# Optimization experiments

Measured on AMD Instinct MI355X. Metric: run time of the kernel, lower is better.

## Reference

```python
import jax, jax.numpy as jnp
import numpy as np

V_F_LEN = 512
I_F_LEN = 256
F_LEN = V_F_LEN + I_F_LEN  # 768, GRU input_size == hidden_size == f_len
NUM_LAYERS = 2
B, S = 64, 256


def _uniform(key, shape, scale):
    return jax.random.uniform(key, shape, jnp.float32, -scale, scale)


def setup_inputs() -> dict:
    key = jax.random.key(0)
    ks = jax.random.split(key, 16)
    fv = jax.random.normal(ks[0], (B, S, V_F_LEN), jnp.float32)
    fi = jax.random.normal(ks[1], (B, S, I_F_LEN), jnp.float32)
    ts = jax.random.uniform(ks[2], (B, S), jnp.float32)
    H = F_LEN
    sc = 1.0 / np.sqrt(H)
    # GRU params, PyTorch layout: [num_layers, 3H, H] with gate order (r, z, n)
    W_ih = _uniform(ks[3], (NUM_LAYERS, 3 * H, H), sc)
    W_hh = _uniform(ks[4], (NUM_LAYERS, 3 * H, H), sc)
    b_ih = _uniform(ks[5], (NUM_LAYERS, 3 * H), sc)
    b_hh = _uniform(ks[6], (NUM_LAYERS, 3 * H), sc)
    sc1 = 1.0 / np.sqrt(H)
    sc2 = 1.0 / np.sqrt(128)
    W1 = _uniform(ks[7], (128, H), sc1)
    b1 = _uniform(ks[8], (128,), sc1)
    W2 = _uniform(ks[9], (6, 128), sc2)
    b2 = _uniform(ks[10], (6,), sc2)
    return {"fv": fv, "fi": fi, "ts": ts, "W_ih": W_ih, "W_hh": W_hh,
            "b_ih": b_ih, "b_hh": b_hh, "W1": W1, "b1": b1, "W2": W2, "b2": b2}


def _gru_layer(x, h0, Wih, Whh, bih, bhh):
    # x: [B, S, H], h0: [B, H]
    def step(h, x_t):
        gi = x_t @ Wih.T + bih          # [B, 3H]
        gh = h @ Whh.T + bhh
        ir, iz, in_ = jnp.split(gi, 3, axis=-1)
        hr, hz, hn = jnp.split(gh, 3, axis=-1)
        r = jax.nn.sigmoid(ir + hr)
        z = jax.nn.sigmoid(iz + hz)
        n = jnp.tanh(in_ + r * hn)
        h_new = (1.0 - z) * n + z * h
        return h_new, h_new
    h_last, ys = jax.lax.scan(step, h0, jnp.swapaxes(x, 0, 1))  # ys: [S, B, H]
    return jnp.swapaxes(ys, 0, 1), h_last


def reference(fv, fi, ts, W_ih, W_hh, b_ih, b_hh, W1, b1, W2, b2):
    # FusionModule with fuse_method='cat': concatenate along feature dim
    fused = jnp.concatenate([fv, fi], axis=-1)  # [B, S, F_LEN]
    bsz = fused.shape[0]
    h0 = jnp.zeros((NUM_LAYERS, bsz, F_LEN), fused.dtype)
    # Note: the torch module feeds one timestep at a time, but the math is
    # identical to running the full sequence through the multilayer GRU.
    x = fused
    h_finals = []
    for l in range(NUM_LAYERS):
        x, h_l = _gru_layer(x, h0[l], W_ih[l], W_hh[l], b_ih[l], b_hh[l])
        h_finals.append(h_l)
    h_n = jnp.stack(h_finals, axis=0)  # [L, B, H]
    hdn = x @ W1.T + b1
    hdn = jnp.where(hdn >= 0, hdn, 0.1 * hdn)  # LeakyReLU(0.1)
    pose = hdn @ W2.T + b2                      # [B, S, 6]
    return (pose, h_n)
```

## Files before the change

kernel.cpp:

```cpp
#include <hip/hip_runtime.h>
#include <stdint.h>


typedef __attribute__((ext_vector_type(8))) short bf16x8;
typedef __attribute__((ext_vector_type(4))) short bf16x4;
typedef __attribute__((ext_vector_type(4))) float f32x4;

#define H_   768
#define TH3  2304
#define BATCH 64
#define SEQ  256
#define SLAB (BATCH * H_)
#define WROW 772
#define FL_ROUND 512

__device__ __forceinline__ uint16_t f2b(float f) {
  union { float f; uint32_t u; } v; v.f = f;
  uint32_t u = v.u;
  return (uint16_t)((u + 0x7FFFu + ((u >> 16) & 1u)) >> 16);
}

__device__ __forceinline__ f32x4 mfma16(bf16x8 a, bf16x8 b, f32x4 c) {
  return __builtin_amdgcn_mfma_f32_16x16x32_bf16(a, b, c, 0, 0, 0);
}

__device__ __forceinline__ bf16x8 ldB(const uint16_t* p) {
  bf16x4 lo = *reinterpret_cast<const bf16x4*>(p);
  bf16x4 hi = *reinterpret_cast<const bf16x4*>(p + 4);
  bf16x8 r;
  r[0] = lo[0]; r[1] = lo[1]; r[2] = lo[2]; r[3] = lo[3];
  r[4] = hi[0]; r[5] = hi[1]; r[6] = hi[2]; r[7] = hi[3];
  return r;
}

__device__ __forceinline__ int fidx(int i, int m, int grp, int slice) {
  return ((i * 2 + m) * 4 + grp) * 64 + slice;
}

__device__ __forceinline__ void pollFlags(const int* base, int lane) {
  const int* fp = base + (lane < 48 ? lane : 0);
  int spins = 0;
  for (;;) {
    int v = __hip_atomic_load(fp, __ATOMIC_RELAXED, __HIP_MEMORY_SCOPE_AGENT);
    if (lane >= 48) v = 1;
    if (__all(v != 0)) break;
    if (++spins > (1 << 15)) break;
    __builtin_amdgcn_s_sleep(1);
  }
  __builtin_amdgcn_sched_barrier(0);
}

__global__ __launch_bounds__(256) void prep_kernel(
    const float* __restrict__ fv, const float* __restrict__ fi,
    const float* __restrict__ W1,
    uint16_t* __restrict__ Xbf, int* __restrict__ flags, uint16_t* __restrict__ W1b)
{
  const int NX = SEQ * SLAB;
  const int NC = 257 * FL_ROUND;
  const int NW = 128 * H_;
  const int total = NX + NC + NW;
  for (int idx = blockIdx.x * blockDim.x + threadIdx.x; idx < total;
       idx += gridDim.x * blockDim.x) {
    if (idx < NX) {
      int s = idx / SLAB;
      int rem = idx - s * SLAB;
      int b = rem / H_;
      int h = rem - b * H_;
      float val = (h < 512) ? fv[((size_t)b * SEQ + s) * 512 + h]
                            : fi[((size_t)b * SEQ + s) * 256 + (h - 512)];
      Xbf[idx] = f2b(val);
    } else if (idx < NX + NC) {
      flags[idx - NX] = 0;
    } else {
      int k = idx - NX - NC;
      W1b[k] = f2b(W1[k]);
    }
  }
}

__global__ __launch_bounds__(256) void gru_persist(
    const float* __restrict__ Wih, const float* __restrict__ Whh,
    const float* __restrict__ bih, const float* __restrict__ bhh,
    const uint16_t* __restrict__ Xbf, uint16_t* __restrict__ Y0, uint16_t* __restrict__ Y1,
    int* __restrict__ flags, float* __restrict__ out_hn)
{
  __shared__ __attribute__((aligned(16))) uint16_t Wx[48 * WROW];
  __shared__ __attribute__((aligned(16))) uint16_t Wh[48 * WROW];
  __shared__ float ghbuf[2][32 * 48];
  __shared__ float hmast[32 * 16];
  __shared__ float bI[48];
  __shared__ float bH[48];

  const int bid   = blockIdx.x;
  const int slice = bid % 48;
  const int layer = (bid / 48) & 1;
  const int bhalf = bid / 96;
  const int grp   = bhalf * 2 + layer;
  const int tid  = threadIdx.x;
  const int lane = tid & 63;
  const int wid  = tid >> 6;
  const int mblk = wid & 1;
  const int isGh = wid >> 1;
  const int n16  = lane & 15;
  const int kg   = lane >> 4;

  const float* wx_g = Wih + (size_t)layer * TH3 * H_;
  const float* wh_g = Whh + (size_t)layer * TH3 * H_;
  for (int idx = tid; idx < 48 * H_; idx += 256) {
    int lr = idx / H_;
    int c  = idx - lr * H_;
    int gate = lr >> 4, j = lr & 15;
    size_t grow = (size_t)(gate * H_ + slice * 16 + j);
    Wx[lr * WROW + c] = f2b(wx_g[grow * H_ + c]);
    Wh[lr * WROW + c] = f2b(wh_g[grow * H_ + c]);
  }
  if (tid < 48) {
    int gate = tid >> 4, j = tid & 15;
    bI[tid] = bih[layer * TH3 + gate * H_ + slice * 16 + j];
    bH[tid] = bhh[layer * TH3 + gate * H_ + slice * 16 + j];
  }
  for (int idx = tid; idx < 32 * 16; idx += 256) hmast[idx] = 0.0f;
  __syncthreads();

  const int batch0 = bhalf * 32;
  uint16_t* Yown = layer ? Y1 : Y0;
  const uint16_t* Wl_h = Wh + (size_t)n16 * WROW + kg * 8;
  const uint16_t* Wl_x = Wx + (size_t)n16 * WROW + kg * 8;

  f32x4 xac0 = {0,0,0,0}, xac1 = {0,0,0,0}, xac2 = {0,0,0,0};

  for (int i = 0; i <= 256; ++i) {
    const bool active = (layer == 0) ? (i < 256) : (i >= 1);
    const bool firstA = (layer == 0) ? (i == 0) : (i == 1);
    float* gb = ghbuf[i & 1];

    if (active) {
      if (isGh) {
        if (firstA) {
          #pragma unroll
          for (int q = 0; q < 4; ++q) {
            int bi = mblk * 16 + 4 * kg + q;
            gb[bi * 48 +      n16] = 0.0f;
            gb[bi * 48 + 16 + n16] = 0.0f;
            gb[bi * 48 + 32 + n16] = 0.0f;
          }
        } else {
          pollFlags(flags + fidx(i - 1, mblk, grp, 0), lane);
          const uint16_t* hs = (layer == 0) ? (Y0 + (size_t)i * SLAB)
                                            : (Y1 + (size_t)(i - 1) * SLAB);
          const uint16_t* ap = hs + (size_t)(batch0 + mblk * 16 + n16) * H_ + kg * 8;
          f32x4 a0 = {0,0,0,0}, a1 = {0,0,0,0}, a2 = {0,0,0,0};
          #pragma unroll
          for (int ks = 0; ks < 24; ++ks) {
            bf16x8 av  = *reinterpret_cast<const bf16x8*>(ap + ks * 32);
            bf16x8 bv0 = ldB(Wl_h + ks * 32);
            bf16x8 bv1 = ldB(Wl_h + 16 * WROW + ks * 32);
            bf16x8 bv2 = ldB(Wl_h + 32 * WROW + ks * 32);
            a0 = mfma16(av, bv0, a0);
            a1 = mfma16(av, bv1, a1);
            a2 = mfma16(av, bv2, a2);
          }
          #pragma unroll
          for (int q = 0; q < 4; ++q) {
            int bi = mblk * 16 + 4 * kg + q;
            gb[bi * 48 +      n16] = a0[q];
            gb[bi * 48 + 16 + n16] = a1[q];
            gb[bi * 48 + 32 + n16] = a2[q];
          }
        }
      } else {
        if (layer == 1) pollFlags(flags + fidx(i - 1, mblk, bhalf * 2, 0), lane);
        const uint16_t* xs = (layer == 0) ? (Xbf + (size_t)i * SLAB)
                                          : (Y0 + (size_t)i * SLAB);
        const uint16_t* ap = xs + (size_t)(batch0 + mblk * 16 + n16) * H_ + kg * 8;
        f32x4 a0 = {0,0,0,0}, a1 = {0,0,0,0}, a2 = {0,0,0,0};
        #pragma unroll
        for (int ks = 0; ks < 24; ++ks) {
          bf16x8 av  = *reinterpret_cast<const bf16x8*>(ap + ks * 32);
          bf16x8 bv0 = ldB(Wl_x + ks * 32);
          bf16x8 bv1 = ldB(Wl_x + 16 * WROW + ks * 32);
          bf16x8 bv2 = ldB(Wl_x + 32 * WROW + ks * 32);
          a0 = mfma16(av, bv0, a0);
          a1 = mfma16(av, bv1, a1);
          a2 = mfma16(av, bv2, a2);
        }
        xac0 = a0; xac1 = a1; xac2 = a2;
      }
    }

    __syncthreads();

    if (active && !isGh) {
      uint16_t* dst = Yown + (size_t)((layer == 0) ? (i + 1) : i) * SLAB;
      const bool lastStep = (layer == 0) ? (i == 255) : (i == 256);
      #pragma unroll
      for (int q = 0; q < 4; ++q) {
        int bi = mblk * 16 + 4 * kg + q;
        float ghr = gb[bi * 48 +      n16] + bH[n16];
        float ghz = gb[bi * 48 + 16 + n16] + bH[16 + n16];
        float ghn = gb[bi * 48 + 32 + n16] + bH[32 + n16];
        float gxr = xac0[q] + bI[n16];
        float gxz = xac1[q] + bI[16 + n16];
        float gxn = xac2[q] + bI[32 + n16];
        float rg = 1.0f / (1.0f + __expf(-(gxr + ghr)));
        float zg = 1.0f / (1.0f + __expf(-(gxz + ghz)));
        float ng = tanhf(gxn + rg * ghn);
        float hv = hmast[bi * 16 + n16];
        float hn2 = (1.0f - zg) * ng + zg * hv;
        hmast[bi * 16 + n16] = hn2;
        uint32_t lo = (uint32_t)f2b(hn2);
        uint32_t partner = (uint32_t)__shfl_xor((int)lo, 1, 64);
        if ((n16 & 1) == 0) {
          uint32_t pack = lo | (partner << 16);
          uint32_t* p = (uint32_t*)(dst + (size_t)(batch0 + bi) * H_ + slice * 16 + n16);
          __hip_atomic_store(p, pack, __ATOMIC_RELAXED, __HIP_MEMORY_SCOPE_AGENT);
        }
        if (lastStep)
          out_hn[(size_t)layer * SLAB + (size_t)(batch0 + bi) * H_ + slice * 16 + n16] = hn2;
      }
      __builtin_amdgcn_s_waitcnt(0);
      __builtin_amdgcn_sched_barrier(0);
      if (lane == 0)
        __hip_atomic_store(&flags[fidx(i, mblk, grp, slice)], 1, __ATOMIC_RELAXED,
                           __HIP_MEMORY_SCOPE_AGENT);
    }
  }
}

__global__ __launch_bounds__(256) void regressor_kernel(
    const uint16_t* __restrict__ Y1, const uint16_t* __restrict__ W1b,
    const float* __restrict__ b1, const float* __restrict__ W2,
    const float* __restrict__ b2, float* __restrict__ pose)
{
  __shared__ float hdn[64 * 132];
  const int t = blockIdx.x;
  const int tid = threadIdx.x;
  const int lane = tid & 63;
  const int wid = tid >> 6;
  const int n16 = lane & 15;
  const int kg = lane >> 4;

  const uint16_t* A  = Y1 + (size_t)(t + 1) * SLAB + (size_t)(wid * 16) * H_;
  const uint16_t* ap = A + (size_t)n16 * H_ + kg * 8;
  const uint16_t* bp = W1b + (size_t)n16 * H_ + kg * 8;

  f32x4 acc[8];
  #pragma unroll
  for (int i = 0; i < 8; ++i) acc[i] = (f32x4){0,0,0,0};

  #pragma unroll
  for (int ks = 0; ks < 24; ++ks) {
    bf16x8 av = *reinterpret_cast<const bf16x8*>(ap + ks * 32);
    #pragma unroll
    for (int nt = 0; nt < 8; ++nt) {
      bf16x8 bv = *reinterpret_cast<const bf16x8*>(bp + (size_t)nt * 16 * H_ + ks * 32);
      acc[nt] = mfma16(av, bv, acc[nt]);
    }
  }
  #pragma unroll
  for (int nt = 0; nt < 8; ++nt) {
    #pragma unroll
    for (int q = 0; q < 4; ++q) {
      int brow = wid * 16 + 4 * kg + q;
      int col  = nt * 16 + n16;
      float v = acc[nt][q] + b1[col];
      v = (v >= 0.0f) ? v : 0.1f * v;
      hdn[brow * 132 + col] = v;
    }
  }
  __syncthreads();
  for (int idx = tid; idx < 384; idx += 256) {
    int b = idx / 6, o = idx % 6;
    const float* w2r = W2 + o * 128;
    const float* hr  = &hdn[b * 132];
    float s = b2[o];
    #pragma unroll 4
    for (int c = 0; c < 128; ++c) s += hr[c] * w2r[c];
    pose[(size_t)b * (SEQ * 6) + (size_t)t * 6 + o] = s;
  }
}

extern "C" void kernel_launch(void* const* d_in, const int* in_sizes, int n_in,
                              void* d_out, int out_size, void* d_ws, size_t ws_size,
                              hipStream_t stream) {
  const float* fv  = (const float*)d_in[0];
  const float* fi  = (const float*)d_in[1];
  const float* Wih = (const float*)d_in[3];
  const float* Whh = (const float*)d_in[4];
  const float* bih = (const float*)d_in[5];
  const float* bhh = (const float*)d_in[6];
  const float* W1  = (const float*)d_in[7];
  const float* b1  = (const float*)d_in[8];
  const float* W2  = (const float*)d_in[9];
  const float* b2  = (const float*)d_in[10];
  float* out = (float*)d_out;

  char* ws = (char*)d_ws;
  size_t off = 0;
  int* flags = (int*)(ws + off);
  off += (size_t)257 * FL_ROUND * sizeof(int);
  off = (off + 255) & ~(size_t)255;
  uint16_t* Xbf = (uint16_t*)(ws + off); off += (size_t)SEQ * SLAB * 2;
  uint16_t* Y0  = (uint16_t*)(ws + off); off += (size_t)257 * SLAB * 2;
  uint16_t* Y1  = (uint16_t*)(ws + off); off += (size_t)257 * SLAB * 2;
  uint16_t* W1b = (uint16_t*)(ws + off); off += (size_t)128 * H_ * 2;

  prep_kernel<<<2048, 256, 0, stream>>>(fv, fi, W1, Xbf, flags, W1b);
  gru_persist<<<192, 256, 0, stream>>>(Wih, Whh, bih, bhh, Xbf, Y0, Y1, flags, out + 98304);
  regressor_kernel<<<SEQ, 256, 0, stream>>>(Y1, W1b, b1, W2, b2, out);
}
```

Baseline: 2.391 ms.

## Pack step flags into bytes, split hidden GEMM along K, use fast tanh

Per-step completion flags become bytes packed into 128-byte groups, so one wave polls all 96 producer slices with two byte loads per lane. Polling no longer sleeps and its spin limit is raised. The recurrent h·Whh GEMM is now split along K across the two Gh waves, each covering both 16-row batch blocks, and the gate stage sums the two partial results. This drops the ghbuf double buffer and reduces the flag wait on the critical path. tanhf is replaced by a clamped exp-based tanh, and removing the double buffer may add a shared-memory hazard between iterations.

Result: slower. 2.510 ms (+5.0%).

```diff
diff --git a/kernel.cpp b/kernel.cpp
--- a/kernel.cpp
+++ b/kernel.cpp
@@ -12,7 +12,7 @@
 #define SEQ  256
 #define SLAB (BATCH * H_)
 #define WROW 772
-#define FL_ROUND 512
+#define FB_ROUND 512
 
 __device__ __forceinline__ uint16_t f2b(float f) {
   union { float f; uint32_t u; } v; v.f = f;
@@ -33,21 +33,43 @@
   return r;
 }
 
-__device__ __forceinline__ int fidx(int i, int m, int grp, int slice) {
-  return ((i * 2 + m) * 4 + grp) * 64 + slice;
-}
-
-__device__ __forceinline__ void pollFlags(const int* base, int lane) {
-  const int* fp = base + (lane < 48 ? lane : 0);
+__device__ __forceinline__ size_t fbIdx(int i, int grp) { return ((size_t)i * 4 + grp) * 128; }
+
+__device__ __forceinline__ uint8_t ldFlag(const uint8_t* p) {
+  return __hip_atomic_load(p, __ATOMIC_RELAXED, __HIP_MEMORY_SCOPE_AGENT);
+}
+
+__device__ __forceinline__ void pollFlags96(const uint8_t* base, int lane) {
+  const uint8_t* p0 = base + lane;
+  const uint8_t* p1 = base + 64 + (lane & 31);
   int spins = 0;
   for (;;) {
-    int v = __hip_atomic_load(fp, __ATOMIC_RELAXED, __HIP_MEMORY_SCOPE_AGENT);
-    if (lane >= 48) v = 1;
-    if (__all(v != 0)) break;
-    if (++spins > (1 << 15)) break;
-    __builtin_amdgcn_s_sleep(1);
+    uint8_t a = ldFlag(p0);
+    uint8_t b = (lane < 32) ? ldFlag(p1) : (uint8_t)1;
+    if (__all(a && b)) break;
+    if (++spins > (1 << 18)) break;
   }
   __builtin_amdgcn_sched_barrier(0);
+}
+
+__device__ __forceinline__ void pollFlags48(const uint8_t* base, int lane) {
+  const uint8_t* p0 = base + (lane < 48 ? lane : 0);
+  int spins = 0;
+  for (;;) {
+    uint8_t a = (lane < 48) ? ldFlag(p0) : (uint8_t)1;
+    if (__all(a)) break;
+    if (++spins > (1 << 18)) break;
+  }
+  __builtin_amdgcn_sched_barrier(0);
+}
+
+__device__ __forceinline__ float fsig(float x) {
+  return 1.0f / (1.0f + __expf(-x));
+}
+__device__ __forceinline__ float ftanh(float x) {
+  x = fminf(fmaxf(x, -15.0f), 15.0f);
+  float e = __expf(2.0f * x);
+  return (e - 1.0f) / (e + 1.0f);
 }
 
 __global__ __launch_bounds__(256) void prep_kernel(
@@ -56,7 +78,7 @@
     uint16_t* __restrict__ Xbf, int* __restrict__ flags, uint16_t* __restrict__ W1b)
 {
   const int NX = SEQ * SLAB;
-  const int NC = 257 * FL_ROUND;
+  const int NC = 257 * FB_ROUND / 4;
   const int NW = 128 * H_;
   const int total = NX + NC + NW;
   for (int idx = blockIdx.x * blockDim.x + threadIdx.x; idx < total;
@@ -82,11 +104,11 @@
     const float* __restrict__ Wih, const float* __restrict__ Whh,
     const float* __restrict__ bih, const float* __restrict__ bhh,
     const uint16_t* __restrict__ Xbf, uint16_t* __restrict__ Y0, uint16_t* __restrict__ Y1,
-    int* __restrict__ flags, float* __restrict__ out_hn)
+    uint8_t* __restrict__ fbytes, float* __restrict__ out_hn)
 {
   __shared__ __attribute__((aligned(16))) uint16_t Wx[48 * WROW];
   __shared__ __attribute__((aligned(16))) uint16_t Wh[48 * WROW];
-  __shared__ float ghbuf[2][32 * 48];
+  __shared__ float ghbuf[2 * 32 * 48];
   __shared__ float hmast[32 * 16];
   __shared__ float bI[48];
   __shared__ float bH[48];
@@ -99,8 +121,9 @@
   const int tid  = threadIdx.x;
   const int lane = tid & 63;
   const int wid  = tid >> 6;
+  const int isGh = wid >> 1;
   const int mblk = wid & 1;
-  const int isGh = wid >> 1;
+  const int kh   = wid & 1;
   const int n16  = lane & 15;
   const int kg   = lane >> 4;
 
@@ -124,52 +147,65 @@
 
   const int batch0 = bhalf * 32;
   uint16_t* Yown = layer ? Y1 : Y0;
-  const uint16_t* Wl_h = Wh + (size_t)n16 * WROW + kg * 8;
-  const uint16_t* Wl_x = Wx + (size_t)n16 * WROW + kg * 8;
+  const uint16_t* Wh_base = Wh + (size_t)n16 * WROW + kg * 8 + kh * 384;
+  const uint16_t* Wx_base = Wx + (size_t)n16 * WROW + kg * 8;
 
   f32x4 xac0 = {0,0,0,0}, xac1 = {0,0,0,0}, xac2 = {0,0,0,0};
 
   for (int i = 0; i <= 256; ++i) {
     const bool active = (layer == 0) ? (i < 256) : (i >= 1);
     const bool firstA = (layer == 0) ? (i == 0) : (i == 1);
-    float* gb = ghbuf[i & 1];
+    float* gb = ghbuf + kh * 1536;
 
     if (active) {
       if (isGh) {
         if (firstA) {
           #pragma unroll
           for (int q = 0; q < 4; ++q) {
-            int bi = mblk * 16 + 4 * kg + q;
-            gb[bi * 48 +      n16] = 0.0f;
-            gb[bi * 48 + 16 + n16] = 0.0f;
-            gb[bi * 48 + 32 + n16] = 0.0f;
+            #pragma unroll
+            for (int m = 0; m < 2; ++m) {
+              int bi = m * 16 + 4 * kg + q;
+              gb[bi * 48 +      n16] = 0.0f;
+              gb[bi * 48 + 16 + n16] = 0.0f;
+              gb[bi * 48 + 32 + n16] = 0.0f;
+            }
           }
         } else {
-          pollFlags(flags + fidx(i - 1, mblk, grp, 0), lane);
+          pollFlags96(fbytes + fbIdx(i - 1, grp), lane);
           const uint16_t* hs = (layer == 0) ? (Y0 + (size_t)i * SLAB)
                                             : (Y1 + (size_t)(i - 1) * SLAB);
-          const uint16_t* ap = hs + (size_t)(batch0 + mblk * 16 + n16) * H_ + kg * 8;
-          f32x4 a0 = {0,0,0,0}, a1 = {0,0,0,0}, a2 = {0,0,0,0};
+          const uint16_t* ap0 = hs + (size_t)(batch0 + n16) * H_ + kh * 384 + kg * 8;
+          const uint16_t* ap1 = ap0 + (size_t)16 * H_;
+          f32x4 a00 = {0,0,0,0}, a01 = {0,0,0,0}, a02 = {0,0,0,0};
+          f32x4 a10 = {0,0,0,0}, a11 = {0,0,0,0}, a12 = {0,0,0,0};
           #pragma unroll
-          for (int ks = 0; ks < 24; ++ks) {
-            bf16x8 av  = *reinterpret_cast<const bf16x8*>(ap + ks * 32);
-            bf16x8 bv0 = ldB(Wl_h + ks * 32);
-            bf16x8 bv1 = ldB(Wl_h + 16 * WROW + ks * 32);
-            bf16x8 bv2 = ldB(Wl_h + 32 * WROW + ks * 32);
-            a0 = mfma16(av, bv0, a0);
-            a1 = mfma16(av, bv1, a1);
-            a2 = mfma16(av, bv2, a2);
+          for (int ks = 0; ks < 12; ++ks) {
+            bf16x8 av0 = *reinterpret_cast<const bf16x8*>(ap0 + ks * 32);
+            bf16x8 av1 = *reinterpret_cast<const bf16x8*>(ap1 + ks * 32);
+            bf16x8 bv0 = ldB(Wh_base + ks * 32);
+            bf16x8 bv1 = ldB(Wh_base + 16 * WROW + ks * 32);
+            bf16x8 bv2 = ldB(Wh_base + 32 * WROW + ks * 32);
+            a00 = mfma16(av0, bv0, a00);
+            a01 = mfma16(av0, bv1, a01);
+            a02 = mfma16(av0, bv2, a02);
+            a10 = mfma16(av1, bv0, a10);
+            a11 = mfma16(av1, bv1, a11);
+            a12 = mfma16(av1, bv2, a12);
           }
           #pragma unroll
           for (int q = 0; q < 4; ++q) {
-            int bi = mblk * 16 + 4 * kg + q;
-            gb[bi * 48 +      n16] = a0[q];
-            gb[bi * 48 + 16 + n16] = a1[q];
-            gb[bi * 48 + 32 + n16] = a2[q];
+            int bi0 = 4 * kg + q;
+            gb[bi0 * 48 +      n16] = a00[q];
+            gb[bi0 * 48 + 16 + n16] = a01[q];
+            gb[bi0 * 48 + 32 + n16] = a02[q];
+            int bi1 = 16 + bi0;
+            gb[bi1 * 48 +      n16] = a10[q];
+            gb[bi1 * 48 + 16 + n16] = a11[q];
+            gb[bi1 * 48 + 32 + n16] = a12[q];
           }
         }
       } else {
-        if (layer == 1) pollFlags(flags + fidx(i - 1, mblk, bhalf * 2, 0), lane);
+        if (layer == 1) pollFlags48(fbytes + fbIdx(i - 1, bhalf * 2) + mblk * 48, lane);
         const uint16_t* xs = (layer == 0) ? (Xbf + (size_t)i * SLAB)
                                           : (Y0 + (size_t)i * SLAB);
         const uint16_t* ap = xs + (size_t)(batch0 + mblk * 16 + n16) * H_ + kg * 8;
@@ -177,9 +213,9 @@
         #pragma unroll
         for (int ks = 0; ks < 24; ++ks) {
           bf16x8 av  = *reinterpret_cast<const bf16x8*>(ap + ks * 32);
-          bf16x8 bv0 = ldB(Wl_x + ks * 32);
-          bf16x8 bv1 = ldB(Wl_x + 16 * WROW + ks * 32);
-          bf16x8 bv2 = ldB(Wl_x + 32 * WROW + ks * 32);
+          bf16x8 bv0 = ldB(Wx_base + ks * 32);
+          bf16x8 bv1 = ldB(Wx_base + 16 * WROW + ks * 32);
+          bf16x8 bv2 = ldB(Wx_base + 32 * WROW + ks * 32);
           a0 = mfma16(av, bv0, a0);
           a1 = mfma16(av, bv1, a1);
           a2 = mfma16(av, bv2, a2);
@@ -196,15 +232,15 @@
       #pragma unroll
       for (int q = 0; q < 4; ++q) {
         int bi = mblk * 16 + 4 * kg + q;
-        float ghr = gb[bi * 48 +      n16] + bH[n16];
-        float ghz = gb[bi * 48 + 16 + n16] + bH[16 + n16];
-        float ghn = gb[bi * 48 + 32 + n16] + bH[32 + n16];
+        float ghr = ghbuf[bi * 48 +      n16] + ghbuf[1536 + bi * 48 +      n16] + bH[n16];
+        float ghz = ghbuf[bi * 48 + 16 + n16] + ghbuf[1536 + bi * 48 + 16 + n16] + bH[16 + n16];
+        float ghn = ghbuf[bi * 48 + 32 + n16] + ghbuf[1536 + bi * 48 + 32 + n16] + bH[32 + n16];
         float gxr = xac0[q] + bI[n16];
         float gxz = xac1[q] + bI[16 + n16];
         float gxn = xac2[q] + bI[32 + n16];
-        float rg = 1.0f / (1.0f + __expf(-(gxr + ghr)));
-        float zg = 1.0f / (1.0f + __expf(-(gxz + ghz)));
-        float ng = tanhf(gxn + rg * ghn);
+        float rg = fsig(gxr + ghr);
+        float zg = fsig(gxz + ghz);
+        float ng = ftanh(gxn + rg * ghn);
         float hv = hmast[bi * 16 + n16];
         float hn2 = (1.0f - zg) * ng + zg * hv;
         hmast[bi * 16 + n16] = hn2;
@@ -221,8 +257,8 @@
       __builtin_amdgcn_s_waitcnt(0);
       __builtin_amdgcn_sched_barrier(0);
       if (lane == 0)
-        __hip_atomic_store(&flags[fidx(i, mblk, grp, slice)], 1, __ATOMIC_RELAXED,
-                           __HIP_MEMORY_SCOPE_AGENT);
+        __hip_atomic_store(fbytes + fbIdx(i, grp) + mblk * 48 + slice, (uint8_t)1,
+                           __ATOMIC_RELAXED, __HIP_MEMORY_SCOPE_AGENT);
     }
   }
 }
@@ -297,15 +333,15 @@
 
   char* ws = (char*)d_ws;
   size_t off = 0;
-  int* flags = (int*)(ws + off);
-  off += (size_t)257 * FL_ROUND * sizeof(int);
+  uint8_t* fbytes = (uint8_t*)(ws + off);
+  off += (size_t)257 * FB_ROUND;
   off = (off + 255) & ~(size_t)255;
   uint16_t* Xbf = (uint16_t*)(ws + off); off += (size_t)SEQ * SLAB * 2;
   uint16_t* Y0  = (uint16_t*)(ws + off); off += (size_t)257 * SLAB * 2;
   uint16_t* Y1  = (uint16_t*)(ws + off); off += (size_t)257 * SLAB * 2;
   uint16_t* W1b = (uint16_t*)(ws + off); off += (size_t)128 * H_ * 2;
 
-  prep_kernel<<<2048, 256, 0, stream>>>(fv, fi, W1, Xbf, flags, W1b);
-  gru_persist<<<192, 256, 0, stream>>>(Wih, Whh, bih, bhh, Xbf, Y0, Y1, flags, out + 98304);
+  prep_kernel<<<2048, 256, 0, stream>>>(fv, fi, W1, Xbf, (int*)fbytes, W1b);
+  gru_persist<<<192, 256, 0, stream>>>(Wih, Whh, bih, bhh, Xbf, Y0, Y1, fbytes, out + 98304);
   regressor_kernel<<<SEQ, 256, 0, stream>>>(Y1, W1b, b1, W2, b2, out);
 }
```

## Merge batch halves into one 512-thread block per slice with block-level flags

Applied to the files above, without the earlier changes.

Each block now handles all 64 batch rows with 8 waves instead of two blocks each doing 32 rows, halving the grid from 192 to 96 blocks. Per-wave flags are replaced by one flag per block, published after a second block-wide barrier. The single-buffered gh scratch is now protected by that barrier, and the hidden state is kept in registers instead of shared memory. Custom fast sigmoid and tanh replace tanhf. This removes duplicated weight staging and cuts the number of flags each poll must check, at the cost of an extra barrier per step and less parallelism across CUs.

Result: no change. 2.348 ms (-1.8%).

```diff
diff --git a/kernel.cpp b/kernel.cpp
--- a/kernel.cpp
+++ b/kernel.cpp
@@ -12,7 +12,7 @@
 #define SEQ  256
 #define SLAB (BATCH * H_)
 #define WROW 772
-#define FL_ROUND 512
+#define FL_STRIDE 128
 
 __device__ __forceinline__ uint16_t f2b(float f) {
   union { float f; uint32_t u; } v; v.f = f;
@@ -33,21 +33,26 @@
   return r;
 }
 
-__device__ __forceinline__ int fidx(int i, int m, int grp, int slice) {
-  return ((i * 2 + m) * 4 + grp) * 64 + slice;
-}
-
-__device__ __forceinline__ void pollFlags(const int* base, int lane) {
+__device__ __forceinline__ void pollFlags48(const int* base, int lane) {
   const int* fp = base + (lane < 48 ? lane : 0);
   int spins = 0;
   for (;;) {
     int v = __hip_atomic_load(fp, __ATOMIC_RELAXED, __HIP_MEMORY_SCOPE_AGENT);
     if (lane >= 48) v = 1;
     if (__all(v != 0)) break;
-    if (++spins > (1 << 15)) break;
+    if (++spins > (1 << 16)) break;
     __builtin_amdgcn_s_sleep(1);
   }
   __builtin_amdgcn_sched_barrier(0);
+}
+
+__device__ __forceinline__ float fsig(float x) {
+  return 1.0f / (1.0f + __expf(-x));
+}
+__device__ __forceinline__ float ftanh(float x) {
+  x = fminf(fmaxf(x, -15.0f), 15.0f);
+  float e = __expf(2.0f * x);
+  return (e - 1.0f) / (e + 1.0f);
 }
 
 __global__ __launch_bounds__(256) void prep_kernel(
@@ -56,7 +61,7 @@
     uint16_t* __restrict__ Xbf, int* __restrict__ flags, uint16_t* __restrict__ W1b)
 {
   const int NX = SEQ * SLAB;
-  const int NC = 257 * FL_ROUND;
+  const int NC = 257 * FL_STRIDE;
   const int NW = 128 * H_;
   const int total = NX + NC + NW;
   for (int idx = blockIdx.x * blockDim.x + threadIdx.x; idx < total;
@@ -78,7 +83,7 @@
   }
 }
 
-__global__ __launch_bounds__(256) void gru_persist(
+__global__ __launch_bounds__(512) void gru_persist(
     const float* __restrict__ Wih, const float* __restrict__ Whh,
     const float* __restrict__ bih, const float* __restrict__ bhh,
     const uint16_t* __restrict__ Xbf, uint16_t* __restrict__ Y0, uint16_t* __restrict__ Y1,
@@ -86,27 +91,24 @@
 {
   __shared__ __attribute__((aligned(16))) uint16_t Wx[48 * WROW];
   __shared__ __attribute__((aligned(16))) uint16_t Wh[48 * WROW];
-  __shared__ float ghbuf[2][32 * 48];
-  __shared__ float hmast[32 * 16];
+  __shared__ float ghbuf[64 * 48];
   __shared__ float bI[48];
   __shared__ float bH[48];
 
   const int bid   = blockIdx.x;
   const int slice = bid % 48;
-  const int layer = (bid / 48) & 1;
-  const int bhalf = bid / 96;
-  const int grp   = bhalf * 2 + layer;
+  const int layer = bid / 48;
   const int tid  = threadIdx.x;
   const int lane = tid & 63;
   const int wid  = tid >> 6;
-  const int mblk = wid & 1;
-  const int isGh = wid >> 1;
+  const int isGh = wid >> 2;
+  const int mblk = wid & 3;
   const int n16  = lane & 15;
   const int kg   = lane >> 4;
 
   const float* wx_g = Wih + (size_t)layer * TH3 * H_;
   const float* wh_g = Whh + (size_t)layer * TH3 * H_;
-  for (int idx = tid; idx < 48 * H_; idx += 256) {
+  for (int idx = tid; idx < 48 * H_; idx += 512) {
     int lr = idx / H_;
     int c  = idx - lr * H_;
     int gate = lr >> 4, j = lr & 15;
@@ -119,20 +121,18 @@
     bI[tid] = bih[layer * TH3 + gate * H_ + slice * 16 + j];
     bH[tid] = bhh[layer * TH3 + gate * H_ + slice * 16 + j];
   }
-  for (int idx = tid; idx < 32 * 16; idx += 256) hmast[idx] = 0.0f;
   __syncthreads();
 
-  const int batch0 = bhalf * 32;
   uint16_t* Yown = layer ? Y1 : Y0;
-  const uint16_t* Wl_h = Wh + (size_t)n16 * WROW + kg * 8;
-  const uint16_t* Wl_x = Wx + (size_t)n16 * WROW + kg * 8;
+  const uint16_t* Wh_base = Wh + (size_t)n16 * WROW + kg * 8;
+  const uint16_t* Wx_base = Wx + (size_t)n16 * WROW + kg * 8;
 
   f32x4 xac0 = {0,0,0,0}, xac1 = {0,0,0,0}, xac2 = {0,0,0,0};
+  float hp[4] = {0.0f, 0.0f, 0.0f, 0.0f};
 
   for (int i = 0; i <= 256; ++i) {
     const bool active = (layer == 0) ? (i < 256) : (i >= 1);
     const bool firstA = (layer == 0) ? (i == 0) : (i == 1);
-    float* gb = ghbuf[i & 1];
 
     if (active) {
       if (isGh) {
@@ -140,22 +140,22 @@
           #pragma unroll
           for (int q = 0; q < 4; ++q) {
             int bi = mblk * 16 + 4 * kg + q;
-            gb[bi * 48 +      n16] = 0.0f;
-            gb[bi * 48 + 16 + n16] = 0.0f;
-            gb[bi * 48 + 32 + n16] = 0.0f;
+            ghbuf[bi * 48 +      n16] = 0.0f;
+            ghbuf[bi * 48 + 16 + n16] = 0.0f;
+            ghbuf[bi * 48 + 32 + n16] = 0.0f;
           }
         } else {
-          pollFlags(flags + fidx(i - 1, mblk, grp, 0), lane);
+          pollFlags48(flags + (size_t)(i - 1) * FL_STRIDE + layer * 64, lane);
           const uint16_t* hs = (layer == 0) ? (Y0 + (size_t)i * SLAB)
                                             : (Y1 + (size_t)(i - 1) * SLAB);
-          const uint16_t* ap = hs + (size_t)(batch0 + mblk * 16 + n16) * H_ + kg * 8;
+          const uint16_t* ap = hs + (size_t)(mblk * 16 + n16) * H_ + kg * 8;
           f32x4 a0 = {0,0,0,0}, a1 = {0,0,0,0}, a2 = {0,0,0,0};
           #pragma unroll
           for (int ks = 0; ks < 24; ++ks) {
             bf16x8 av  = *reinterpret_cast<const bf16x8*>(ap + ks * 32);
-            bf16x8 bv0 = ldB(Wl_h + ks * 32);
-            bf16x8 bv1 = ldB(Wl_h + 16 * WROW + ks * 32);
-            bf16x8 bv2 = ldB(Wl_h + 32 * WROW + ks * 32);
+            bf16x8 bv0 = ldB(Wh_base + ks * 32);
+            bf16x8 bv1 = ldB(Wh_base + 16 * WROW + ks * 32);
+            bf16x8 bv2 = ldB(Wh_base + 32 * WROW + ks * 32);
             a0 = mfma16(av, bv0, a0);
             a1 = mfma16(av, bv1, a1);
             a2 = mfma16(av, bv2, a2);
@@ -163,23 +163,23 @@
           #pragma unroll
           for (int q = 0; q < 4; ++q) {
             int bi = mblk * 16 + 4 * kg + q;
-            gb[bi * 48 +      n16] = a0[q];
-            gb[bi * 48 + 16 + n16] = a1[q];
-            gb[bi * 48 + 32 + n16] = a2[q];
+            ghbuf[bi * 48 +      n16] = a0[q];
+            ghbuf[bi * 48 + 16 + n16] = a1[q];
+            ghbuf[bi * 48 + 32 + n16] = a2[q];
           }
         }
       } else {
-        if (layer == 1) pollFlags(flags + fidx(i - 1, mblk, bhalf * 2, 0), lane);
+        if (layer == 1) pollFlags48(flags + (size_t)(i - 1) * FL_STRIDE, lane);
         const uint16_t* xs = (layer == 0) ? (Xbf + (size_t)i * SLAB)
                                           : (Y0 + (size_t)i * SLAB);
-        const uint16_t* ap = xs + (size_t)(batch0 + mblk * 16 + n16) * H_ + kg * 8;
+        const uint16_t* ap = xs + (size_t)(mblk * 16 + n16) * H_ + kg * 8;
         f32x4 a0 = {0,0,0,0}, a1 = {0,0,0,0}, a2 = {0,0,0,0};
         #pragma unroll
         for (int ks = 0; ks < 24; ++ks) {
           bf16x8 av  = *reinterpret_cast<const bf16x8*>(ap + ks * 32);
-          bf16x8 bv0 = ldB(Wl_x + ks * 32);
-          bf16x8 bv1 = ldB(Wl_x + 16 * WROW + ks * 32);
-          bf16x8 bv2 = ldB(Wl_x + 32 * WROW + ks * 32);
+          bf16x8 bv0 = ldB(Wx_base + ks * 32);
+          bf16x8 bv1 = ldB(Wx_base + 16 * WROW + ks * 32);
+          bf16x8 bv2 = ldB(Wx_base + 32 * WROW + ks * 32);
           a0 = mfma16(av, bv0, a0);
           a1 = mfma16(av, bv1, a1);
           a2 = mfma16(av, bv2, a2);
@@ -187,7 +187,6 @@
         xac0 = a0; xac1 = a1; xac2 = a2;
       }
     }
-
     __syncthreads();
 
     if (active && !isGh) {
@@ -196,34 +195,36 @@
       #pragma unroll
       for (int q = 0; q < 4; ++q) {
         int bi = mblk * 16 + 4 * kg + q;
-        float ghr = gb[bi * 48 +      n16] + bH[n16];
-        float ghz = gb[bi * 48 + 16 + n16] + bH[16 + n16];
-        float ghn = gb[bi * 48 + 32 + n16] + bH[32 + n16];
+        float ghr = ghbuf[bi * 48 +      n16] + bH[n16];
+        float ghz = ghbuf[bi * 48 + 16 + n16] + bH[16 + n16];
+        float ghn = ghbuf[bi * 48 + 32 + n16] + bH[32 + n16];
         float gxr = xac0[q] + bI[n16];
         float gxz = xac1[q] + bI[16 + n16];
         float gxn = xac2[q] + bI[32 + n16];
-        float rg = 1.0f / (1.0f + __expf(-(gxr + ghr)));
-        float zg = 1.0f / (1.0f + __expf(-(gxz + ghz)));
-        float ng = tanhf(gxn + rg * ghn);
-        float hv = hmast[bi * 16 + n16];
-        float hn2 = (1.0f - zg) * ng + zg * hv;
-        hmast[bi * 16 + n16] = hn2;
+        float rg = fsig(gxr + ghr);
+        float zg = fsig(gxz + ghz);
+        float ng = ftanh(gxn + rg * ghn);
+        float hn2 = (1.0f - zg) * ng + zg * hp[q];
+        hp[q] = hn2;
         uint32_t lo = (uint32_t)f2b(hn2);
         uint32_t partner = (uint32_t)__shfl_xor((int)lo, 1, 64);
         if ((n16 & 1) == 0) {
           uint32_t pack = lo | (partner << 16);
-          uint32_t* p = (uint32_t*)(dst + (size_t)(batch0 + bi) * H_ + slice * 16 + n16);
+          uint32_t* p = (uint32_t*)(dst + (size_t)bi * H_ + slice * 16 + n16);
           __hip_atomic_store(p, pack, __ATOMIC_RELAXED, __HIP_MEMORY_SCOPE_AGENT);
         }
         if (lastStep)
-          out_hn[(size_t)layer * SLAB + (size_t)(batch0 + bi) * H_ + slice * 16 + n16] = hn2;
+          out_hn[(size_t)layer * SLAB + (size_t)bi * H_ + slice * 16 + n16] = hn2;
       }
       __builtin_amdgcn_s_waitcnt(0);
       __builtin_amdgcn_sched_barrier(0);
-      if (lane == 0)
-        __hip_atomic_store(&flags[fidx(i, mblk, grp, slice)], 1, __ATOMIC_RELAXED,
-                           __HIP_MEMORY_SCOPE_AGENT);
-    }
+    }
+
+    __syncthreads();
+
+    if (i < 256 && tid == 0)
+      __hip_atomic_store(&flags[(size_t)i * FL_STRIDE + layer * 64 + slice], 1,
+                         __ATOMIC_RELAXED, __HIP_MEMORY_SCOPE_AGENT);
   }
 }
 
@@ -298,7 +299,7 @@
   char* ws = (char*)d_ws;
   size_t off = 0;
   int* flags = (int*)(ws + off);
-  off += (size_t)257 * FL_ROUND * sizeof(int);
+  off += (size_t)257 * FL_STRIDE * sizeof(int);
   off = (off + 255) & ~(size_t)255;
   uint16_t* Xbf = (uint16_t*)(ws + off); off += (size_t)SEQ * SLAB * 2;
   uint16_t* Y0  = (uint16_t*)(ws + off); off += (size_t)257 * SLAB * 2;
@@ -306,6 +307,6 @@
   uint16_t* W1b = (uint16_t*)(ws + off); off += (size_t)128 * H_ * 2;
 
   prep_kernel<<<2048, 256, 0, stream>>>(fv, fi, W1, Xbf, flags, W1b);
-  gru_persist<<<192, 256, 0, stream>>>(Wih, Whh, bih, bhh, Xbf, Y0, Y1, flags, out + 98304);
+  gru_persist<<<96, 512, 0, stream>>>(Wih, Whh, bih, bhh, Xbf, Y0, Y1, flags, out + 98304);
   regressor_kernel<<<SEQ, 256, 0, stream>>>(Y1, W1b, b1, W2, b2, out);
 }
```
